# Performance work log

Measured on AMD Instinct MI355X. Metric: run time of the kernel, lower is better.

## Reference

```python
import jax, jax.numpy as jnp
import numpy as np

B, S, D, H = 4, 2048, 1024, 16
HD = D // H  # head_dim = 64


def setup_inputs() -> dict:
    key = jax.random.key(0)
    ks = jax.random.split(key, 5)
    scale = 1.0 / np.sqrt(D)  # xavier-ish
    return {
        "query": jax.random.normal(ks[0], (B, S, D), dtype=jnp.float32),
        "Wq": jax.random.normal(ks[1], (D, D), dtype=jnp.float32) * scale,
        "bq": jnp.zeros((D,), dtype=jnp.float32),
        "Wk": jax.random.normal(ks[2], (D, D), dtype=jnp.float32) * scale,
        "bk": jnp.zeros((D,), dtype=jnp.float32),
        "Wv": jax.random.normal(ks[3], (D, D), dtype=jnp.float32) * scale,
        "bv": jnp.zeros((D,), dtype=jnp.float32),
        "Wo": jax.random.normal(ks[4], (D, D), dtype=jnp.float32) * scale,
        "bo": jnp.zeros((D,), dtype=jnp.float32),
    }


def reference(query, Wq, bq, Wk, bk, Wv, bv, Wo, bo):
    # Self-attention: key = value = query. Linear layers use y = x @ W^T + b (torch nn.Linear).
    q = query @ Wq.T + bq
    k = query @ Wk.T + bk
    v = query @ Wv.T + bv
    # [B, S, D] -> [B, H, S, HD]
    q = q.reshape(B, S, H, HD).transpose(0, 2, 1, 3)
    k = k.reshape(B, S, H, HD).transpose(0, 2, 1, 3)
    v = v.reshape(B, S, H, HD).transpose(0, 2, 1, 3)
    scores = jnp.einsum('bhqd,bhkd->bhqk', q, k) / jnp.sqrt(jnp.float32(HD))
    attn = jax.nn.softmax(scores, axis=-1)  # dropout=0 (eval)
    out = jnp.einsum('bhqk,bhkd->bhqd', attn, v)
    out = out.transpose(0, 2, 1, 3).reshape(B, S, D)
    out = out @ Wo.T + bo
    return out
```

## Files before the change

kernel.cpp:

```cpp
#include <hip/hip_runtime.h>
#include <cstdint>


#define B_ 4
#define S_ 2048
#define D_ 1024
#define H_ 16
#define HD_ 64
#define QKV_N 3072
#define SCALE_Q 0.18033688011111772f

typedef __bf16 bf16x8 __attribute__((ext_vector_type(8)));
typedef float f32x4 __attribute__((ext_vector_type(4)));
typedef short short8 __attribute__((ext_vector_type(8)));

__device__ __forceinline__ unsigned short f2bf(float f) {
  unsigned int u = __builtin_bit_cast(unsigned int, f);
  u = (u + 0x7FFFu + ((u >> 16) & 1u)) >> 16;
  return (unsigned short)u;
}

__device__ __forceinline__ void gload16(const void* g, void* l) {
  __builtin_amdgcn_global_load_lds(
      (const __attribute__((address_space(1))) void*)g,
      (__attribute__((address_space(3))) void*)l, 16, 0, 0);
}

__global__ __launch_bounds__(256) void cvt_bf16(const float* __restrict__ in,
                                                unsigned short* __restrict__ out, int n8) {
  int i = blockIdx.x * 256 + threadIdx.x;
  if (i >= n8) return;
  const float4* p = (const float4*)in + (size_t)i * 2;
  float4 a = p[0], b = p[1];
  unsigned short o[8] = {f2bf(a.x), f2bf(a.y), f2bf(a.z), f2bf(a.w),
                         f2bf(b.x), f2bf(b.y), f2bf(b.z), f2bf(b.w)};
  *(uint4*)(out + (size_t)i * 8) = *(const uint4*)o;
}

__global__ __launch_bounds__(256) void cvt_w4(const float* __restrict__ w0, const float* __restrict__ w1,
                                              const float* __restrict__ w2, const float* __restrict__ w3,
                                              unsigned short* __restrict__ dst) {
  int y = blockIdx.y;
  const float* src = (y == 0) ? w0 : (y == 1) ? w1 : (y == 2) ? w2 : w3;
  float s = (y == 0) ? SCALE_Q : 1.0f;
  int i = blockIdx.x * 256 + threadIdx.x;
  const float4* p = (const float4*)src + (size_t)i * 2;
  float4 a = p[0], b = p[1];
  unsigned short o[8] = {f2bf(a.x * s), f2bf(a.y * s), f2bf(a.z * s), f2bf(a.w * s),
                         f2bf(b.x * s), f2bf(b.y * s), f2bf(b.z * s), f2bf(b.w * s)};
  *(uint4*)(dst + (size_t)y * 1048576 + (size_t)i * 8) = *(const uint4*)o;
}

__global__ __launch_bounds__(256) void bias_cat(const float* __restrict__ bq, const float* __restrict__ bk,
                                                const float* __restrict__ bv, float* __restrict__ bcat) {
  int i = blockIdx.x * 256 + threadIdx.x;
  float v = (i < 1024) ? bq[i] * SCALE_Q : (i < 2048) ? bk[i - 1024] : bv[i - 2048];
  bcat[i] = v;
}

__global__ __launch_bounds__(256) void gemm_bt(
    const unsigned short* __restrict__ A, const unsigned short* __restrict__ W,
    const float* __restrict__ bias, void* __restrict__ Cout,
    int M, int N, int K, int out_bf16) {
  __shared__ __attribute__((aligned(16))) unsigned short sA[128 * 32];
  __shared__ __attribute__((aligned(16))) unsigned short sB[128 * 32];
  const int t = threadIdx.x;
  const int lane = t & 63;
  const int w = t >> 6;
  const int lm = lane & 15;
  const int quad = lane >> 4;
  const int m0 = blockIdx.y * 128;
  const int n0 = blockIdx.x * 128;
  const int wm = (w & 1) * 64;
  const int wn = (w >> 1) * 64;

  const int off0 = t * 8, off1 = t * 8 + 2048;
  const int ar0 = off0 >> 5, ac0 = (((off0 >> 3) & 3) ^ ((ar0 >> 1) & 3)) * 8;
  const int ar1 = off1 >> 5, ac1 = (((off1 >> 3) & 3) ^ ((ar1 >> 1) & 3)) * 8;
  const unsigned short* Ag0 = A + (size_t)(m0 + ar0) * K + ac0;
  const unsigned short* Ag1 = A + (size_t)(m0 + ar1) * K + ac1;
  const unsigned short* Wg0 = W + (size_t)(n0 + ar0) * K + ac0;
  const unsigned short* Wg1 = W + (size_t)(n0 + ar1) * K + ac1;
  unsigned short* sA0 = &sA[w * 512];
  unsigned short* sA1 = &sA[2048 + w * 512];
  unsigned short* sB0 = &sB[w * 512];
  unsigned short* sB1 = &sB[2048 + w * 512];

  f32x4 acc[4][4] = {};

  for (int kt = 0; kt < K; kt += 32) {
    gload16(Ag0 + kt, sA0);
    gload16(Ag1 + kt, sA1);
    gload16(Wg0 + kt, sB0);
    gload16(Wg1 + kt, sB1);
    __syncthreads();
    bf16x8 af[4], bf[4];
#pragma unroll
    for (int mi = 0; mi < 4; ++mi) {
      int row = wm + mi * 16 + lm;
      af[mi] = *(const bf16x8*)&sA[row * 32 + ((quad ^ ((row >> 1) & 3)) << 3)];
    }
#pragma unroll
    for (int ni = 0; ni < 4; ++ni) {
      int row = wn + ni * 16 + lm;
      bf[ni] = *(const bf16x8*)&sB[row * 32 + ((quad ^ ((row >> 1) & 3)) << 3)];
    }
#pragma unroll
    for (int mi = 0; mi < 4; ++mi)
#pragma unroll
      for (int ni = 0; ni < 4; ++ni)
        acc[mi][ni] = __builtin_amdgcn_mfma_f32_16x16x32_bf16(af[mi], bf[ni], acc[mi][ni], 0, 0, 0);
    __syncthreads();
  }

#pragma unroll
  for (int mi = 0; mi < 4; ++mi)
#pragma unroll
    for (int ni = 0; ni < 4; ++ni) {
      int col = n0 + wn + ni * 16 + lm;
      float bv = bias[col];
#pragma unroll
      for (int r = 0; r < 4; ++r) {
        int row = m0 + wm + mi * 16 + quad * 4 + r;
        float v = acc[mi][ni][r] + bv;
        if (out_bf16)
          ((unsigned short*)Cout)[(size_t)row * N + col] = f2bf(v);
        else
          ((float*)Cout)[(size_t)row * N + col] = v;
      }
    }
}

__global__ __launch_bounds__(256) void transpose_v(const unsigned short* __restrict__ qkv,
                                                   unsigned short* __restrict__ vt) {
  __shared__ unsigned short tile[64][72];
  const int t = threadIdx.x;
  const int bh = blockIdx.y;
  const int b = bh >> 4, h = bh & 15;
  const int s0 = blockIdx.x * 64;
#pragma unroll
  for (int r = 0; r < 2; ++r) {
    int idx = t + r * 256;
    int row = idx >> 3;
    int c = idx & 7;
    uint4 d = *(const uint4*)(qkv + (size_t)(b * S_ + s0 + row) * QKV_N + 2048 + h * HD_ + c * 8);
    const unsigned short* ds = (const unsigned short*)&d;
#pragma unroll
    for (int j = 0; j < 8; ++j) tile[row][c * 8 + j] = ds[j];
  }
  __syncthreads();
#pragma unroll
  for (int r = 0; r < 2; ++r) {
    int idx = t + r * 256;
    int hd = idx >> 3;
    int sc = idx & 7;
    unsigned short o[8];
#pragma unroll
    for (int j = 0; j < 8; ++j) o[j] = tile[sc * 8 + j][hd];
    *(uint4*)(vt + (size_t)bh * HD_ * S_ + (size_t)hd * S_ + s0 + sc * 8) = *(const uint4*)o;
  }
}

__global__ __launch_bounds__(256, 2) void attn_kernel(
    const unsigned short* __restrict__ qkv, const unsigned short* __restrict__ vt,
    unsigned short* __restrict__ ab) {
  __shared__ __attribute__((aligned(16))) unsigned short sK[2][64 * 64];
  __shared__ __attribute__((aligned(16))) unsigned short sV[2][64 * 64];
  __shared__ __attribute__((aligned(16))) unsigned short sP[4][64 * 64];

  const int t = threadIdx.x;
  const int lane = t & 63;
  const int w = t >> 6;
  const int lm = lane & 15;
  const int quad = lane >> 4;
  const int bh = blockIdx.y;
  const int b = bh >> 4, h = bh & 15;
  const int q0 = blockIdx.x * 256;

  const unsigned short* qg = qkv + (size_t)b * S_ * QKV_N + h * HD_;
  const unsigned short* kg = qg + 1024;
  const unsigned short* vg = vt + (size_t)bh * HD_ * S_;

  const int off0 = t * 8, off1 = off0 + 2048;
  const int r0 = off0 >> 6, c0 = (((off0 >> 3) & 7) ^ (r0 & 7)) * 8;
  const int r1 = off1 >> 6, c1 = (((off1 >> 3) & 7) ^ (r1 & 7)) * 8;

  gload16(kg + (size_t)r0 * QKV_N + c0, &sK[0][w * 512]);
  gload16(kg + (size_t)r1 * QKV_N + c1, &sK[0][2048 + w * 512]);
  gload16(vg + (size_t)r0 * S_ + c0, &sV[0][w * 512]);
  gload16(vg + (size_t)r1 * S_ + c1, &sV[0][2048 + w * 512]);

  bf16x8 qf[4][2];
#pragma unroll
  for (int mi = 0; mi < 4; ++mi) {
    int row = q0 + w * 64 + mi * 16 + lm;
#pragma unroll
    for (int kc = 0; kc < 2; ++kc)
      qf[mi][kc] = *(const bf16x8*)(qg + (size_t)row * QKV_N + kc * 32 + quad * 8);
  }
  __syncthreads();

  unsigned short* sPw = sP[w];
  const bf16x8 ones = __builtin_bit_cast(bf16x8, (short8)(short)0x3F80);
  f32x4 o[4][4] = {};
  f32x4 Lacc[4] = {};

  for (int n0 = 0; n0 < S_; n0 += 64) {
    const int cur = (n0 >> 6) & 1, nxt = cur ^ 1;
    if (n0 + 64 < S_) {
      gload16(kg + (size_t)(n0 + 64 + r0) * QKV_N + c0, &sK[nxt][w * 512]);
      gload16(kg + (size_t)(n0 + 64 + r1) * QKV_N + c1, &sK[nxt][2048 + w * 512]);
      gload16(vg + (size_t)r0 * S_ + (n0 + 64) + c0, &sV[nxt][w * 512]);
      gload16(vg + (size_t)r1 * S_ + (n0 + 64) + c1, &sV[nxt][2048 + w * 512]);
    }

    f32x4 s[4][4] = {};
#pragma unroll
    for (int kc = 0; kc < 2; ++kc)
#pragma unroll
      for (int nb = 0; nb < 4; ++nb) {
        int row = nb * 16 + lm;
        bf16x8 kf = *(const bf16x8*)&sK[cur][row * 64 + (((kc * 4 + quad) ^ (row & 7)) << 3)];
#pragma unroll
        for (int mi = 0; mi < 4; ++mi)
          s[mi][nb] = __builtin_amdgcn_mfma_f32_16x16x32_bf16(kf, qf[mi][kc], s[mi][nb], 0, 0, 0);
      }

#pragma unroll
    for (int mi = 0; mi < 4; ++mi) {
      int prow = mi * 16 + lm;
      char* rowp = (char*)sPw + prow * 128;
#pragma unroll
      for (int nb = 0; nb < 4; ++nb) {
        const f32x4& sv = s[mi][nb];
        unsigned int u0 = (__builtin_bit_cast(unsigned int, __builtin_amdgcn_exp2f(sv[0])) + 0x8000u) >> 16;
        unsigned int u1 = (__builtin_bit_cast(unsigned int, __builtin_amdgcn_exp2f(sv[1])) + 0x8000u) >> 16;
        unsigned int u2 = (__builtin_bit_cast(unsigned int, __builtin_amdgcn_exp2f(sv[2])) + 0x8000u) >> 16;
        unsigned int u3 = (__builtin_bit_cast(unsigned int, __builtin_amdgcn_exp2f(sv[3])) + 0x8000u) >> 16;
        uint2 pk = {u0 | (u1 << 16), u2 | (u3 << 16)};
        int c16 = (nb * 2 + (quad >> 1)) ^ (prow & 7);
        *(uint2*)(rowp + (c16 << 4) + ((quad & 1) << 3)) = pk;
      }
    }

#pragma unroll
    for (int kc = 0; kc < 2; ++kc) {
      bf16x8 pf[4];
#pragma unroll
      for (int mi = 0; mi < 4; ++mi) {
        int prow = mi * 16 + lm;
        pf[mi] = *(const bf16x8*)&sPw[prow * 64 + (((kc * 4 + quad) ^ (prow & 7)) << 3)];
        Lacc[mi] = __builtin_amdgcn_mfma_f32_16x16x32_bf16(pf[mi], ones, Lacc[mi], 0, 0, 0);
      }
#pragma unroll
      for (int nf = 0; nf < 4; ++nf) {
        int row = nf * 16 + lm;
        bf16x8 vf = *(const bf16x8*)&sV[cur][row * 64 + (((kc * 4 + quad) ^ (row & 7)) << 3)];
#pragma unroll
        for (int mi = 0; mi < 4; ++mi)
          o[mi][nf] = __builtin_amdgcn_mfma_f32_16x16x32_bf16(pf[mi], vf, o[mi][nf], 0, 0, 0);
      }
    }
    __syncthreads();
  }

#pragma unroll
  for (int mi = 0; mi < 4; ++mi)
#pragma unroll
    for (int r = 0; r < 4; ++r) {
      float rinv = 1.0f / Lacc[mi][r];
      int row = q0 + w * 64 + mi * 16 + quad * 4 + r;
#pragma unroll
      for (int nf = 0; nf < 4; ++nf) {
        int col = h * HD_ + nf * 16 + lm;
        ab[(size_t)(b * S_ + row) * D_ + col] = f2bf(o[mi][nf][r] * rinv);
      }
    }
}

extern "C" void kernel_launch(void* const* d_in, const int* in_sizes, int n_in,
                              void* d_out, int out_size, void* d_ws, size_t ws_size,
                              hipStream_t stream) {
  const float* x = (const float*)d_in[0];
  const float* Wq = (const float*)d_in[1];
  const float* bq = (const float*)d_in[2];
  const float* Wk = (const float*)d_in[3];
  const float* bk = (const float*)d_in[4];
  const float* Wv = (const float*)d_in[5];
  const float* bv = (const float*)d_in[6];
  const float* Wo = (const float*)d_in[7];
  const float* bo = (const float*)d_in[8];
  float* out = (float*)d_out;

  const size_t E = (size_t)B_ * S_ * D_;
  const size_t WE = (size_t)D_ * D_;
  unsigned short* xb = (unsigned short*)d_ws;
  unsigned short* wcat = xb + E;
  unsigned short* wob = wcat + 3 * WE;
  float* bcat = (float*)(wcat + 4 * WE);
  unsigned short* qkv = (unsigned short*)(bcat + 4096);
  unsigned short* vtb = qkv + (size_t)B_ * S_ * QKV_N;
  unsigned short* abuf = xb;

  cvt_bf16<<<dim3((unsigned)(E / 8 / 256)), 256, 0, stream>>>(x, xb, (int)(E / 8));
  cvt_w4<<<dim3(512, 4), 256, 0, stream>>>(Wq, Wk, Wv, Wo, wcat);
  bias_cat<<<dim3(12), 256, 0, stream>>>(bq, bk, bv, bcat);

  gemm_bt<<<dim3(QKV_N / 128, (B_ * S_) / 128), 256, 0, stream>>>(
      xb, wcat, bcat, qkv, B_ * S_, QKV_N, D_, 1);
  transpose_v<<<dim3(S_ / 64, B_ * H_), 256, 0, stream>>>(qkv, vtb);
  attn_kernel<<<dim3(S_ / 256, B_ * H_), 256, 0, stream>>>(qkv, vtb, abuf);
  gemm_bt<<<dim3(D_ / 128, (B_ * S_) / 128), 256, 0, stream>>>(
      abuf, wob, bo, out, B_ * S_, D_, D_, 0);
}
```

Measured before the change: 301.0 us.

## Fuse V transpose into QKV GEMM epilogue and reorder block grids

The QKV GEMM epilogue now writes Q and K into a compact 2048-wide buffer and writes V directly in transposed per-head layout, so the separate transpose_v kernel and its extra pass over V are gone. The GEMM grid is swapped so M tiles vary fastest, and the attention grid is flattened so all heads for one query block are adjacent, changing cache locality of weight and K/V reuse. Softmax probabilities use the hardware bf16 pack conversion instead of manual rounding. The transposed V stores are 8-byte scattered writes with stride S, which may be less coalesced than the old transpose kernel.

Measured after the change: 275.7 us. -8.4%, faster.

```diff
diff --git a/kernel.cpp b/kernel.cpp
--- a/kernel.cpp
+++ b/kernel.cpp
@@ -8,9 +8,11 @@
 #define H_ 16
 #define HD_ 64
 #define QKV_N 3072
+#define QK_LD 2048
 #define SCALE_Q 0.18033688011111772f
 
 typedef __bf16 bf16x8 __attribute__((ext_vector_type(8)));
+typedef __bf16 bf16x2 __attribute__((ext_vector_type(2)));
 typedef float f32x4 __attribute__((ext_vector_type(4)));
 typedef short short8 __attribute__((ext_vector_type(8)));
 
@@ -18,6 +20,13 @@
   unsigned int u = __builtin_bit_cast(unsigned int, f);
   u = (u + 0x7FFFu + ((u >> 16) & 1u)) >> 16;
   return (unsigned short)u;
+}
+
+__device__ __forceinline__ unsigned int pkbf(float a, float b) {
+  bf16x2 v;
+  v.x = (__bf16)a;
+  v.y = (__bf16)b;
+  return __builtin_bit_cast(unsigned int, v);
 }
 
 __device__ __forceinline__ void gload16(const void* g, void* l) {
@@ -61,7 +70,7 @@
 __global__ __launch_bounds__(256) void gemm_bt(
     const unsigned short* __restrict__ A, const unsigned short* __restrict__ W,
     const float* __restrict__ bias, void* __restrict__ Cout,
-    int M, int N, int K, int out_bf16) {
+    unsigned short* __restrict__ vt, int M, int N, int K, int mode) {
   __shared__ __attribute__((aligned(16))) unsigned short sA[128 * 32];
   __shared__ __attribute__((aligned(16))) unsigned short sB[128 * 32];
   const int t = threadIdx.x;
@@ -69,8 +78,8 @@
   const int w = t >> 6;
   const int lm = lane & 15;
   const int quad = lane >> 4;
-  const int m0 = blockIdx.y * 128;
-  const int n0 = blockIdx.x * 128;
+  const int m0 = blockIdx.x * 128;
+  const int n0 = blockIdx.y * 128;
   const int wm = (w & 1) * 64;
   const int wn = (w >> 1) * 64;
 
@@ -119,50 +128,34 @@
     for (int ni = 0; ni < 4; ++ni) {
       int col = n0 + wn + ni * 16 + lm;
       float bv = bias[col];
-#pragma unroll
-      for (int r = 0; r < 4; ++r) {
-        int row = m0 + wm + mi * 16 + quad * 4 + r;
-        float v = acc[mi][ni][r] + bv;
-        if (out_bf16)
-          ((unsigned short*)Cout)[(size_t)row * N + col] = f2bf(v);
-        else
-          ((float*)Cout)[(size_t)row * N + col] = v;
-      }
-    }
-}
-
-__global__ __launch_bounds__(256) void transpose_v(const unsigned short* __restrict__ qkv,
-                                                   unsigned short* __restrict__ vt) {
-  __shared__ unsigned short tile[64][72];
-  const int t = threadIdx.x;
-  const int bh = blockIdx.y;
-  const int b = bh >> 4, h = bh & 15;
-  const int s0 = blockIdx.x * 64;
-#pragma unroll
-  for (int r = 0; r < 2; ++r) {
-    int idx = t + r * 256;
-    int row = idx >> 3;
-    int c = idx & 7;
-    uint4 d = *(const uint4*)(qkv + (size_t)(b * S_ + s0 + row) * QKV_N + 2048 + h * HD_ + c * 8);
-    const unsigned short* ds = (const unsigned short*)&d;
-#pragma unroll
-    for (int j = 0; j < 8; ++j) tile[row][c * 8 + j] = ds[j];
-  }
-  __syncthreads();
-#pragma unroll
-  for (int r = 0; r < 2; ++r) {
-    int idx = t + r * 256;
-    int hd = idx >> 3;
-    int sc = idx & 7;
-    unsigned short o[8];
-#pragma unroll
-    for (int j = 0; j < 8; ++j) o[j] = tile[sc * 8 + j][hd];
-    *(uint4*)(vt + (size_t)bh * HD_ * S_ + (size_t)hd * S_ + s0 + sc * 8) = *(const uint4*)o;
-  }
+      float v0 = acc[mi][ni][0] + bv, v1 = acc[mi][ni][1] + bv;
+      float v2 = acc[mi][ni][2] + bv, v3 = acc[mi][ni][3] + bv;
+      int rbase = m0 + wm + mi * 16 + quad * 4;
+      if (mode == 0) {
+        float* op = (float*)Cout;
+        op[(size_t)(rbase + 0) * N + col] = v0;
+        op[(size_t)(rbase + 1) * N + col] = v1;
+        op[(size_t)(rbase + 2) * N + col] = v2;
+        op[(size_t)(rbase + 3) * N + col] = v3;
+      } else if (col < 2048) {
+        unsigned short* op = (unsigned short*)Cout;
+        op[(size_t)(rbase + 0) * QK_LD + col] = f2bf(v0);
+        op[(size_t)(rbase + 1) * QK_LD + col] = f2bf(v1);
+        op[(size_t)(rbase + 2) * QK_LD + col] = f2bf(v2);
+        op[(size_t)(rbase + 3) * QK_LD + col] = f2bf(v3);
+      } else {
+        int c = col - 2048;
+        int bh = (m0 >> 11) * 16 + (c >> 6);
+        int hd = c & 63;
+        int sbase = (rbase & 2047);
+        uint2 pk = {pkbf(v0, v1), pkbf(v2, v3)};
+        *(uint2*)(vt + (size_t)bh * (HD_ * S_) + (size_t)hd * S_ + sbase) = pk;
+      }
+    }
 }
 
 __global__ __launch_bounds__(256, 2) void attn_kernel(
-    const unsigned short* __restrict__ qkv, const unsigned short* __restrict__ vt,
+    const unsigned short* __restrict__ qk, const unsigned short* __restrict__ vt,
     unsigned short* __restrict__ ab) {
   __shared__ __attribute__((aligned(16))) unsigned short sK[2][64 * 64];
   __shared__ __attribute__((aligned(16))) unsigned short sV[2][64 * 64];
@@ -173,11 +166,11 @@
   const int w = t >> 6;
   const int lm = lane & 15;
   const int quad = lane >> 4;
-  const int bh = blockIdx.y;
+  const int bh = blockIdx.x & 63;
   const int b = bh >> 4, h = bh & 15;
-  const int q0 = blockIdx.x * 256;
-
-  const unsigned short* qg = qkv + (size_t)b * S_ * QKV_N + h * HD_;
+  const int q0 = (blockIdx.x >> 6) * 256;
+
+  const unsigned short* qg = qk + (size_t)b * S_ * QK_LD + h * HD_;
   const unsigned short* kg = qg + 1024;
   const unsigned short* vg = vt + (size_t)bh * HD_ * S_;
 
@@ -185,8 +178,8 @@
   const int r0 = off0 >> 6, c0 = (((off0 >> 3) & 7) ^ (r0 & 7)) * 8;
   const int r1 = off1 >> 6, c1 = (((off1 >> 3) & 7) ^ (r1 & 7)) * 8;
 
-  gload16(kg + (size_t)r0 * QKV_N + c0, &sK[0][w * 512]);
-  gload16(kg + (size_t)r1 * QKV_N + c1, &sK[0][2048 + w * 512]);
+  gload16(kg + (size_t)r0 * QK_LD + c0, &sK[0][w * 512]);
+  gload16(kg + (size_t)r1 * QK_LD + c1, &sK[0][2048 + w * 512]);
   gload16(vg + (size_t)r0 * S_ + c0, &sV[0][w * 512]);
   gload16(vg + (size_t)r1 * S_ + c1, &sV[0][2048 + w * 512]);
 
@@ -196,7 +189,7 @@
     int row = q0 + w * 64 + mi * 16 + lm;
 #pragma unroll
     for (int kc = 0; kc < 2; ++kc)
-      qf[mi][kc] = *(const bf16x8*)(qg + (size_t)row * QKV_N + kc * 32 + quad * 8);
+      qf[mi][kc] = *(const bf16x8*)(qg + (size_t)row * QK_LD + kc * 32 + quad * 8);
   }
   __syncthreads();
 
@@ -208,8 +201,8 @@
   for (int n0 = 0; n0 < S_; n0 += 64) {
     const int cur = (n0 >> 6) & 1, nxt = cur ^ 1;
     if (n0 + 64 < S_) {
-      gload16(kg + (size_t)(n0 + 64 + r0) * QKV_N + c0, &sK[nxt][w * 512]);
-      gload16(kg + (size_t)(n0 + 64 + r1) * QKV_N + c1, &sK[nxt][2048 + w * 512]);
+      gload16(kg + (size_t)(n0 + 64 + r0) * QK_LD + c0, &sK[nxt][w * 512]);
+      gload16(kg + (size_t)(n0 + 64 + r1) * QK_LD + c1, &sK[nxt][2048 + w * 512]);
       gload16(vg + (size_t)r0 * S_ + (n0 + 64) + c0, &sV[nxt][w * 512]);
       gload16(vg + (size_t)r1 * S_ + (n0 + 64) + c1, &sV[nxt][2048 + w * 512]);
     }
@@ -233,11 +226,8 @@
 #pragma unroll
       for (int nb = 0; nb < 4; ++nb) {
         const f32x4& sv = s[mi][nb];
-        unsigned int u0 = (__builtin_bit_cast(unsigned int, __builtin_amdgcn_exp2f(sv[0])) + 0x8000u) >> 16;
-        unsigned int u1 = (__builtin_bit_cast(unsigned int, __builtin_amdgcn_exp2f(sv[1])) + 0x8000u) >> 16;
-        unsigned int u2 = (__builtin_bit_cast(unsigned int, __builtin_amdgcn_exp2f(sv[2])) + 0x8000u) >> 16;
-        unsigned int u3 = (__builtin_bit_cast(unsigned int, __builtin_amdgcn_exp2f(sv[3])) + 0x8000u) >> 16;
-        uint2 pk = {u0 | (u1 << 16), u2 | (u3 << 16)};
+        uint2 pk = {pkbf(__builtin_amdgcn_exp2f(sv[0]), __builtin_amdgcn_exp2f(sv[1])),
+                    pkbf(__builtin_amdgcn_exp2f(sv[2]), __builtin_amdgcn_exp2f(sv[3]))};
         int c16 = (nb * 2 + (quad >> 1)) ^ (prow & 7);
         *(uint2*)(rowp + (c16 << 4) + ((quad & 1) << 3)) = pk;
       }
@@ -298,18 +288,17 @@
   unsigned short* wcat = xb + E;
   unsigned short* wob = wcat + 3 * WE;
   float* bcat = (float*)(wcat + 4 * WE);
-  unsigned short* qkv = (unsigned short*)(bcat + 4096);
-  unsigned short* vtb = qkv + (size_t)B_ * S_ * QKV_N;
+  unsigned short* qkb = (unsigned short*)(bcat + 4096);
+  unsigned short* vtb = qkb + (size_t)B_ * S_ * QK_LD;
   unsigned short* abuf = xb;
 
   cvt_bf16<<<dim3((unsigned)(E / 8 / 256)), 256, 0, stream>>>(x, xb, (int)(E / 8));
   cvt_w4<<<dim3(512, 4), 256, 0, stream>>>(Wq, Wk, Wv, Wo, wcat);
   bias_cat<<<dim3(12), 256, 0, stream>>>(bq, bk, bv, bcat);
 
-  gemm_bt<<<dim3(QKV_N / 128, (B_ * S_) / 128), 256, 0, stream>>>(
-      xb, wcat, bcat, qkv, B_ * S_, QKV_N, D_, 1);
-  transpose_v<<<dim3(S_ / 64, B_ * H_), 256, 0, stream>>>(qkv, vtb);
-  attn_kernel<<<dim3(S_ / 256, B_ * H_), 256, 0, stream>>>(qkv, vtb, abuf);
-  gemm_bt<<<dim3(D_ / 128, (B_ * S_) / 128), 256, 0, stream>>>(
-      abuf, wob, bo, out, B_ * S_, D_, D_, 0);
-}
+  gemm_bt<<<dim3((B_ * S_) / 128, QKV_N / 128), 256, 0, stream>>>(
+      xb, wcat, bcat, qkb, vtb, B_ * S_, QKV_N, D_, 1);
+  attn_kernel<<<dim3(512), 256, 0, stream>>>(qkb, vtb, abuf);
+  gemm_bt<<<dim3((B_ * S_) / 128, D_ / 128), 256, 0, stream>>>(
+      abuf, wob, bo, out, nullptr, B_ * S_, D_, D_, 0);
+}
```
